# Kernel optimization log

Hardware: AMD Instinct MI355X
Metric: run time of the kernel (lower is better)

The kernel has to match this reference:

```python
import jax, jax.numpy as jnp
import numpy as np

B, K, M, D = 2048, 64, 64, 256
NI, EPS, MI = 15, 0.05, 3


def setup_inputs() -> dict:
    key = jax.random.key(0)
    ks = jax.random.split(key, 8)
    sq = jax.random.normal(ks[0], (B, K, D), dtype=jnp.float32)
    sr = jax.random.normal(ks[1], (B, M, D), dtype=jnp.float32)
    mq = jax.random.uniform(ks[2], (B, K), dtype=jnp.float32)
    mr = jax.random.uniform(ks[3], (B, M), dtype=jnp.float32)
    scale = 1.0 / np.sqrt(D)
    W1 = jax.random.normal(ks[4], (D, D), dtype=jnp.float32) * scale
    b1 = jnp.zeros((D,), dtype=jnp.float32)
    W2 = jax.random.normal(ks[5], (D, D), dtype=jnp.float32) * scale
    b2 = jnp.zeros((D,), dtype=jnp.float32)
    return {"sq": sq, "sr": sr, "mq": mq, "mr": mr,
            "W1": W1, "b1": b1, "W2": W2, "b2": b2}


def _mlp(x, W1, b1, W2, b2):
    # nn.Linear: x @ W.T + b
    h = jax.nn.relu(jnp.einsum('bnd,ed->bne', x, W1) + b1)
    return jnp.einsum('bnd,ed->bne', h, W2) + b2


def _cdist(x, y):
    # Euclidean pairwise distance [B,K,M]
    x2 = jnp.sum(x * x, -1)[:, :, None]
    y2 = jnp.sum(y * y, -1)[:, None, :]
    xy = jnp.einsum('bkd,bmd->bkm', x, y)
    return jnp.sqrt(jnp.clip(x2 + y2 - 2.0 * xy, 0.0))


def reference(sq, sr, mq, mr, W1, b1, W2, b2):
    fq = _mlp(sq, W1, b1, W2, b2)
    fr = _mlp(sr, W1, b1, W2, b2)
    C = _cdist(fq, fr)                                   # [B,K,M]
    lK = (-C / EPS
          + jnp.log(jnp.clip(mq, 1e-8))[:, :, None]
          + jnp.log(jnp.clip(mr, 1e-8))[:, None, :])

    la0 = jnp.zeros((B, K, 1), dtype=C.dtype)
    lb0 = jnp.zeros((B, 1, M), dtype=C.dtype)

    def sink_body(_, carry):
        la, lb = carry
        la = -jax.nn.logsumexp(lK + lb, axis=2, keepdims=True)
        lb = -jax.nn.logsumexp(lK + la, axis=1, keepdims=True)
        return (la, lb)

    la, lb = jax.lax.fori_loop(0, NI, sink_body, (la0, lb0))
    T = jnp.exp(lK + la + lb)

    def pow_body(_, T):
        T = T * T
        T = T / (jnp.sum(T, -1, keepdims=True) + 1e-8)
        T = T / (jnp.sum(T, -2, keepdims=True) + 1e-8)
        return T

    T = jax.lax.fori_loop(0, MI, pow_body, T)
    c = jnp.sum(T * C, axis=(-1, -2))                    # [B]
    return (jax.nn.sigmoid(-c), T, C, c)
```

## Files before the change

### kernel.cpp

```cpp
#include <hip/hip_runtime.h>
#include <math.h>

#define NB    2048
#define KK    64
#define MM    64
#define DD    256
#define NITER 15
#define MITER 3
#define IEPS  20.0f

typedef __bf16 bf16_t;
typedef bf16_t bf16x8 __attribute__((ext_vector_type(8)));
typedef bf16_t bf16x4 __attribute__((ext_vector_type(4)));
typedef float  f32x16 __attribute__((ext_vector_type(16)));

#define XSTR 264
#define CSTR 65

#define F_BYTES   134217728ull
#define WBF_ELEMS 131072

__global__ __launch_bounds__(256) void convert_w(const float* __restrict__ W1,
                                                 const float* __restrict__ W2,
                                                 bf16_t* __restrict__ wbf) {
    int i = blockIdx.x * 256 + threadIdx.x;
    if (i < 65536) wbf[i] = (bf16_t)W1[i];
    else           wbf[i] = (bf16_t)W2[i - 65536];
}

__device__ __forceinline__ void mlp_layer64(const bf16_t* __restrict__ in,
                                            const bf16_t* __restrict__ W,
                                            const float*  __restrict__ bias,
                                            bf16_t* __restrict__ outLds,
                                            bool relu, int l31, int lh, int wv) {
    #pragma unroll
    for (int etp = 0; etp < 2; ++etp) {
        const int e0 = (wv * 2 + etp) * 32;
        bf16x8 af[16];
        const bf16_t* wrow = W + (size_t)(e0 + l31) * 256 + lh * 8;
        #pragma unroll
        for (int kc = 0; kc < 16; ++kc) af[kc] = *(const bf16x8*)(wrow + kc * 16);

        const bf16_t* x0 = in + (size_t)l31 * XSTR + lh * 8;
        const bf16_t* x1 = x0 + 32 * XSTR;
        f32x16 a[2];
        #pragma unroll
        for (int i = 0; i < 16; ++i) { a[0][i] = 0.0f; a[1][i] = 0.0f; }
        #pragma unroll
        for (int kc = 0; kc < 16; ++kc) {
            bf16x8 bx0 = *(const bf16x8*)(x0 + kc * 16);
            bf16x8 bx1 = *(const bf16x8*)(x1 + kc * 16);
            a[0] = __builtin_amdgcn_mfma_f32_32x32x16_bf16(af[kc], bx0, a[0], 0, 0, 0);
            a[1] = __builtin_amdgcn_mfma_f32_32x32x16_bf16(af[kc], bx1, a[1], 0, 0, 0);
        }
        #pragma unroll
        for (int z = 0; z < 2; ++z) {
            const int n = z * 32 + l31;
            #pragma unroll
            for (int g = 0; g < 4; ++g) {
                const int e = e0 + 8 * g + 4 * lh;
                bf16x4 p;
                #pragma unroll
                for (int rr = 0; rr < 4; ++rr) {
                    float v = a[z][4 * g + rr] + bias[e + rr];
                    if (relu) v = fmaxf(v, 0.0f);
                    p[rr] = (bf16_t)v;
                }
                *(bf16x4*)&outLds[(size_t)n * XSTR + e] = p;
            }
        }
    }
}

__global__ __launch_bounds__(256, 2) void mlp_pair(
    const float* __restrict__ sq, const float* __restrict__ sr,
    const float* __restrict__ b1, const float* __restrict__ b2,
    const bf16_t* __restrict__ wbf, bf16_t* __restrict__ fout) {

    __shared__ bf16_t Xs[64 * XSTR];
    __shared__ bf16_t Hs[64 * XSTR];
    __shared__ float  b1_s[256], b2_s[256];

    const int bi = blockIdx.x;
    const int t  = threadIdx.x;
    const int ln = t & 63;
    const int wv = t >> 6;
    const int l31 = ln & 31;
    const int lh  = ln >> 5;

    const int b = bi >> 1, half = bi & 1;
    const float4* s4 = (const float4*)((half ? sr : sq) + (size_t)b * 64 * 256);

    #pragma unroll
    for (int it = 0; it < 16; ++it) {
        const int i  = t + it * 256;
        const int r  = i >> 6;
        const int c4 = i & 63;
        float4 v = s4[i];
        bf16x4 p;
        p[0] = (bf16_t)v.x; p[1] = (bf16_t)v.y;
        p[2] = (bf16_t)v.z; p[3] = (bf16_t)v.w;
        *(bf16x4*)&Xs[(size_t)r * XSTR + c4 * 4] = p;
    }
    b1_s[t] = b1[t];
    b2_s[t] = b2[t];
    __syncthreads();

    mlp_layer64(Xs, wbf, b1_s, Hs, true, l31, lh, wv);
    __syncthreads();
    mlp_layer64(Hs, wbf + 65536, b2_s, Xs, false, l31, lh, wv);
    __syncthreads();

    bf16_t* fg = fout + (size_t)bi * 64 * 256;
    #pragma unroll
    for (int it = 0; it < 8; ++it) {
        const int i = t + it * 256;
        const int r = i >> 5;
        const int c = i & 31;
        bf16x8 v = *(const bf16x8*)&Xs[(size_t)r * XSTR + c * 8];
        *(bf16x8*)&fg[(size_t)r * 256 + c * 8] = v;
    }
}

__global__ __launch_bounds__(256, 2) void sinkhorn_ot(
    const bf16_t* __restrict__ fg,
    const float* __restrict__ mq, const float* __restrict__ mr,
    float* __restrict__ out) {

    __shared__ __align__(16) char smem[128 * XSTR * 2];
    bf16_t* Fs = (bf16_t*)smem;
    float*  Cs = (float*)smem;
    float*  Ts = (float*)(smem + 64 * CSTR * 4);
    __shared__ float nrm[128];
    __shared__ float lmq_s[64], lmr_s[64], la_s[64], lb_s[64];
    __shared__ float red_s[4];

    const int b  = blockIdx.x;
    const int t  = threadIdx.x;
    const int ln = t & 63;
    const int wv = t >> 6;
    const int l31 = ln & 31;
    const int lh  = ln >> 5;

    {
        const bf16_t* fb = fg + (size_t)b * 128 * 256;
        #pragma unroll
        for (int it = 0; it < 16; ++it) {
            const int i = t + it * 256;
            const int r = i >> 5;
            const int c = i & 31;
            bf16x8 v = *(const bf16x8*)&fb[(size_t)r * 256 + c * 8];
            *(bf16x8*)&Fs[(size_t)r * XSTR + c * 8] = v;
        }
        if (t < 64)        lmq_s[t]      = __logf(fmaxf(mq[(size_t)b * 64 + t], 1e-8f));
        else if (t < 128)  lmr_s[t - 64] = __logf(fmaxf(mr[(size_t)b * 64 + (t - 64)], 1e-8f));
        else if (t < 192)  lb_s[t - 128] = 0.0f;
    }
    __syncthreads();

    {
        const int r  = t >> 1;
        const int hf = t & 1;
        const bf16_t* frow = &Fs[(size_t)r * XSTR + hf * 128];
        float s = 0.0f;
        #pragma unroll
        for (int c = 0; c < 16; ++c) {
            bf16x8 v = *(const bf16x8*)(frow + c * 8);
            #pragma unroll
            for (int j2 = 0; j2 < 8; ++j2) { float f = (float)v[j2]; s = fmaf(f, f, s); }
        }
        s += __shfl_xor(s, 1);
        if (hf == 0) nrm[r] = s;
    }
    __syncthreads();

    float cvv[16];
    int   qbase, mcol;
    {
        const int qt = wv >> 1, rt = wv & 1;
        const bf16_t* qa = &Fs[(size_t)(qt * 32 + l31) * XSTR + lh * 8];
        const bf16_t* ra = &Fs[(size_t)(64 + rt * 32 + l31) * XSTR + lh * 8];
        f32x16 acc;
        #pragma unroll
        for (int i = 0; i < 16; ++i) acc[i] = 0.0f;
        #pragma unroll
        for (int kc = 0; kc < 16; ++kc) {
            bf16x8 av = *(const bf16x8*)(qa + kc * 16);
            bf16x8 bv = *(const bf16x8*)(ra + kc * 16);
            acc = __builtin_amdgcn_mfma_f32_32x32x16_bf16(av, bv, acc, 0, 0, 0);
        }
        float* outC = out + 2048 + (size_t)2048 * 4096 + (size_t)b * 4096;
        mcol = rt * 32 + l31;
        qbase = qt * 32;
        const float nr_m = nrm[64 + mcol];
        #pragma unroll
        for (int g = 0; g < 4; ++g) {
            #pragma unroll
            for (int rr = 0; rr < 4; ++rr) {
                const int q = qbase + 8 * g + 4 * lh + rr;
                float d2 = nrm[q] + nr_m - 2.0f * acc[4 * g + rr];
                float cv = sqrtf(fmaxf(d2, 0.0f));
                cvv[4 * g + rr] = cv;
                outC[q * 64 + mcol] = cv;
            }
        }
    }
    __syncthreads();
    {
        #pragma unroll
        for (int g = 0; g < 4; ++g) {
            #pragma unroll
            for (int rr = 0; rr < 4; ++rr) {
                const int q = qbase + 8 * g + 4 * lh + rr;
                Cs[q * CSTR + mcol] = cvv[4 * g + rr];
            }
        }
    }
    __syncthreads();

    const int ki = t >> 2;
    const int jj = t & 3;
    float rowV[16], colV[16];
    #pragma unroll
    for (int i = 0; i < 16; ++i) {
        const int m2 = jj * 16 + i;
        rowV[i] = fmaf(Cs[ki * CSTR + m2], -IEPS, lmr_s[m2]);
        colV[i] = fmaf(Cs[m2 * CSTR + ki], -IEPS, lmq_s[m2]);
    }
    const float lmq_k = lmq_s[ki];
    const float lmr_m = lmr_s[ki];
    float vals[16];

    for (int it = 0; it < NITER; ++it) {
        float mx = -1e30f;
        #pragma unroll
        for (int i = 0; i < 16; ++i) {
            float v = rowV[i] + lb_s[jj * 16 + i];
            vals[i] = v; mx = fmaxf(mx, v);
        }
        mx = fmaxf(mx, __shfl_xor(mx, 1));
        mx = fmaxf(mx, __shfl_xor(mx, 2));
        float s = 0.0f;
        #pragma unroll
        for (int i = 0; i < 16; ++i) s += __expf(vals[i] - mx);
        s += __shfl_xor(s, 1);
        s += __shfl_xor(s, 2);
        if (jj == 0) la_s[ki] = -(lmq_k + mx + __logf(s));
        __syncthreads();

        mx = -1e30f;
        #pragma unroll
        for (int i = 0; i < 16; ++i) {
            float v = colV[i] + la_s[jj * 16 + i];
            vals[i] = v; mx = fmaxf(mx, v);
        }
        mx = fmaxf(mx, __shfl_xor(mx, 1));
        mx = fmaxf(mx, __shfl_xor(mx, 2));
        s = 0.0f;
        #pragma unroll
        for (int i = 0; i < 16; ++i) s += __expf(vals[i] - mx);
        s += __shfl_xor(s, 1);
        s += __shfl_xor(s, 2);
        if (jj == 0) lb_s[ki] = -(lmr_m + mx + __logf(s));
        __syncthreads();
    }

    {
        const float base = lmq_k + la_s[ki];
        #pragma unroll
        for (int i = 0; i < 16; ++i) {
            const int m2 = jj * 16 + i;
            Ts[ki * CSTR + m2] = __expf(rowV[i] + lb_s[m2] + base);
        }
    }
    __syncthreads();

    for (int pi = 0; pi < MITER; ++pi) {
        float vv[16], rs = 0.0f;
        #pragma unroll
        for (int i = 0; i < 16; ++i) {
            float v = Ts[ki * CSTR + jj * 16 + i];
            v = v * v; vv[i] = v; rs += v;
        }
        rs += __shfl_xor(rs, 1); rs += __shfl_xor(rs, 2);
        float inv = 1.0f / (rs + 1e-8f);
        #pragma unroll
        for (int i = 0; i < 16; ++i) Ts[ki * CSTR + jj * 16 + i] = vv[i] * inv;
        __syncthreads();

        float cs = 0.0f;
        #pragma unroll
        for (int i = 0; i < 16; ++i) { float v = Ts[(jj * 16 + i) * CSTR + ki]; vv[i] = v; cs += v; }
        cs += __shfl_xor(cs, 1); cs += __shfl_xor(cs, 2);
        inv = 1.0f / (cs + 1e-8f);
        #pragma unroll
        for (int i = 0; i < 16; ++i) Ts[(jj * 16 + i) * CSTR + ki] = vv[i] * inv;
        __syncthreads();
    }

    {
        float part = 0.0f;
        float tq[16];
        #pragma unroll
        for (int i = 0; i < 16; ++i) {
            const int m2 = jj * 16 + i;
            float tv = Ts[ki * CSTR + m2];
            tq[i] = tv;
            part = fmaf(tv, Cs[ki * CSTR + m2], part);
        }
        float* outT = out + 2048 + (size_t)b * 4096 + ki * 64 + jj * 16;
        #pragma unroll
        for (int q4 = 0; q4 < 4; ++q4) {
            ((float4*)outT)[q4] = make_float4(tq[4 * q4], tq[4 * q4 + 1],
                                              tq[4 * q4 + 2], tq[4 * q4 + 3]);
        }
        #pragma unroll
        for (int off = 1; off < 64; off <<= 1) part += __shfl_xor(part, off);
        if (ln == 0) red_s[wv] = part;
    }
    __syncthreads();
    if (t == 0) {
        float c = red_s[0] + red_s[1] + red_s[2] + red_s[3];
        out[2048 + (size_t)2 * 2048 * 4096 + b] = c;
        out[b] = 1.0f / (1.0f + __expf(c));
    }
}

__device__ __forceinline__ void mlp_layer128(const bf16_t* __restrict__ in,
                                             const bf16_t* __restrict__ W,
                                             const float*  __restrict__ bias,
                                             bf16_t* __restrict__ outLds,
                                             bool relu, int ln, int wv) {
    const int l31 = ln & 31;
    const int lh  = ln >> 5;
    for (int etp = 0; etp < 2; ++etp) {
        const int e0 = (wv * 2 + etp) * 32;
        bf16x8 af[16];
        const bf16_t* wrow = W + (size_t)(e0 + l31) * 256 + lh * 8;
        #pragma unroll
        for (int kc = 0; kc < 16; ++kc) af[kc] = *(const bf16x8*)(wrow + kc * 16);
        #pragma unroll
        for (int ntp = 0; ntp < 2; ++ntp) {
            const bf16_t* x0 = in + (size_t)(ntp * 64 + l31) * XSTR + lh * 8;
            const bf16_t* x1 = x0 + 32 * XSTR;
            f32x16 a[2];
            #pragma unroll
            for (int i = 0; i < 16; ++i) { a[0][i] = 0.0f; a[1][i] = 0.0f; }
            #pragma unroll
            for (int kc = 0; kc < 16; ++kc) {
                bf16x8 bx0 = *(const bf16x8*)(x0 + kc * 16);
                bf16x8 bx1 = *(const bf16x8*)(x1 + kc * 16);
                a[0] = __builtin_amdgcn_mfma_f32_32x32x16_bf16(af[kc], bx0, a[0], 0, 0, 0);
                a[1] = __builtin_amdgcn_mfma_f32_32x32x16_bf16(af[kc], bx1, a[1], 0, 0, 0);
            }
            #pragma unroll
            for (int z = 0; z < 2; ++z) {
                const int n = ntp * 64 + z * 32 + l31;
                #pragma unroll
                for (int g = 0; g < 4; ++g) {
                    const int e = e0 + 8 * g + 4 * lh;
                    bf16x4 p;
                    #pragma unroll
                    for (int rr = 0; rr < 4; ++rr) {
                        float v = a[z][4 * g + rr] + bias[e + rr];
                        if (relu) v = fmaxf(v, 0.0f);
                        p[rr] = (bf16_t)v;
                    }
                    *(bf16x4*)&outLds[(size_t)n * XSTR + e] = p;
                }
            }
        }
    }
}

__global__ __launch_bounds__(256, 1) void sinkhorn_fused(
    const float* __restrict__ sq, const float* __restrict__ sr,
    const float* __restrict__ mq, const float* __restrict__ mr,
    const float* __restrict__ b1, const float* __restrict__ b2,
    const bf16_t* __restrict__ wbf,
    float* __restrict__ out) {

    __shared__ bf16_t Xs[128 * XSTR];
    __shared__ bf16_t Hs[128 * XSTR];
    __shared__ float  Cs[64 * CSTR];
    __shared__ float  nrm[128];
    __shared__ float  lmq_s[64], lmr_s[64], la_s[64], lb_s[64];
    __shared__ float  b1_s[256], b2_s[256];
    __shared__ float  red_s[4];

    const int b  = blockIdx.x;
    const int t  = threadIdx.x;
    const int ln = t & 63;
    const int wv = t >> 6;
    const int l31 = ln & 31;
    const int lh  = ln >> 5;

    {
        const float4* sq4 = (const float4*)(sq + (size_t)b * KK * DD);
        const float4* sr4 = (const float4*)(sr + (size_t)b * MM * DD);
        for (int i = t; i < 8192; i += 256) {
            const int r  = i >> 6;
            const int c4 = i & 63;
            float4 v = (r < 64) ? sq4[r * 64 + c4] : sr4[(r - 64) * 64 + c4];
            bf16x4 p;
            p[0] = (bf16_t)v.x; p[1] = (bf16_t)v.y;
            p[2] = (bf16_t)v.z; p[3] = (bf16_t)v.w;
            *(bf16x4*)&Xs[(size_t)r * XSTR + c4 * 4] = p;
        }
        b1_s[t] = b1[t];
        b2_s[t] = b2[t];
        if (t < 64)        lmq_s[t]       = __logf(fmaxf(mq[(size_t)b * 64 + t], 1e-8f));
        else if (t < 128)  lmr_s[t - 64]  = __logf(fmaxf(mr[(size_t)b * 64 + (t - 64)], 1e-8f));
        else if (t < 192)  lb_s[t - 128]  = 0.0f;
    }
    __syncthreads();
    mlp_layer128(Xs, wbf, b1_s, Hs, true, ln, wv);
    __syncthreads();
    mlp_layer128(Hs, wbf + 65536, b2_s, Xs, false, ln, wv);
    __syncthreads();
    {
        const int r  = t >> 1;
        const int hf = t & 1;
        const bf16_t* frow = &Xs[(size_t)r * XSTR + hf * 128];
        float s = 0.0f;
        #pragma unroll
        for (int c = 0; c < 16; ++c) {
            bf16x8 v = *(const bf16x8*)(frow + c * 8);
            #pragma unroll
            for (int j2 = 0; j2 < 8; ++j2) { float f = (float)v[j2]; s = fmaf(f, f, s); }
        }
        s += __shfl_xor(s, 1);
        if (hf == 0) nrm[r] = s;
    }
    __syncthreads();
    {
        const int qt = wv >> 1, rt = wv & 1;
        const bf16_t* qa = &Xs[(size_t)(qt * 32 + l31) * XSTR + lh * 8];
        const bf16_t* ra = &Xs[(size_t)(64 + rt * 32 + l31) * XSTR + lh * 8];
        f32x16 acc;
        #pragma unroll
        for (int i = 0; i < 16; ++i) acc[i] = 0.0f;
        #pragma unroll
        for (int kc = 0; kc < 16; ++kc) {
            bf16x8 av = *(const bf16x8*)(qa + kc * 16);
            bf16x8 bv = *(const bf16x8*)(ra + kc * 16);
            acc = __builtin_amdgcn_mfma_f32_32x32x16_bf16(av, bv, acc, 0, 0, 0);
        }
        float* outC = out + 2048 + (size_t)2048 * 4096 + (size_t)b * 4096;
        const int m = rt * 32 + l31;
        const float nr_m = nrm[64 + m];
        #pragma unroll
        for (int g = 0; g < 4; ++g) {
            #pragma unroll
            for (int rr = 0; rr < 4; ++rr) {
                const int q = qt * 32 + 8 * g + 4 * lh + rr;
                float d2 = nrm[q] + nr_m - 2.0f * acc[4 * g + rr];
                float cv = sqrtf(fmaxf(d2, 0.0f));
                Cs[q * CSTR + m] = cv;
                outC[q * 64 + m] = cv;
            }
        }
    }
    __syncthreads();

    const int ki = t >> 2;
    const int jj = t & 3;
    float rowV[16], colV[16];
    #pragma unroll
    for (int i = 0; i < 16; ++i) {
        const int m2 = jj * 16 + i;
        rowV[i] = fmaf(Cs[ki * CSTR + m2], -IEPS, lmr_s[m2]);
        colV[i] = fmaf(Cs[m2 * CSTR + ki], -IEPS, lmq_s[m2]);
    }
    const float lmq_k = lmq_s[ki];
    const float lmr_m = lmr_s[ki];
    float vals[16];

    for (int it = 0; it < NITER; ++it) {
        float mx = -1e30f;
        #pragma unroll
        for (int i = 0; i < 16; ++i) {
            float v = rowV[i] + lb_s[jj * 16 + i];
            vals[i] = v; mx = fmaxf(mx, v);
        }
        mx = fmaxf(mx, __shfl_xor(mx, 1));
        mx = fmaxf(mx, __shfl_xor(mx, 2));
        float s = 0.0f;
        #pragma unroll
        for (int i = 0; i < 16; ++i) s += __expf(vals[i] - mx);
        s += __shfl_xor(s, 1);
        s += __shfl_xor(s, 2);
        if (jj == 0) la_s[ki] = -(lmq_k + mx + __logf(s));
        __syncthreads();

        mx = -1e30f;
        #pragma unroll
        for (int i = 0; i < 16; ++i) {
            float v = colV[i] + la_s[jj * 16 + i];
            vals[i] = v; mx = fmaxf(mx, v);
        }
        mx = fmaxf(mx, __shfl_xor(mx, 1));
        mx = fmaxf(mx, __shfl_xor(mx, 2));
        s = 0.0f;
        #pragma unroll
        for (int i = 0; i < 16; ++i) s += __expf(vals[i] - mx);
        s += __shfl_xor(s, 1);
        s += __shfl_xor(s, 2);
        if (jj == 0) lb_s[ki] = -(lmr_m + mx + __logf(s));
        __syncthreads();
    }

    float* Ts = (float*)Hs;
    {
        const float base = lmq_k + la_s[ki];
        #pragma unroll
        for (int i = 0; i < 16; ++i) {
            const int m2 = jj * 16 + i;
            Ts[ki * CSTR + m2] = __expf(rowV[i] + lb_s[m2] + base);
        }
    }
    __syncthreads();

    for (int pi = 0; pi < MITER; ++pi) {
        float vv[16], rs = 0.0f;
        #pragma unroll
        for (int i = 0; i < 16; ++i) {
            float v = Ts[ki * CSTR + jj * 16 + i];
            v = v * v; vv[i] = v; rs += v;
        }
        rs += __shfl_xor(rs, 1); rs += __shfl_xor(rs, 2);
        float inv = 1.0f / (rs + 1e-8f);
        #pragma unroll
        for (int i = 0; i < 16; ++i) Ts[ki * CSTR + jj * 16 + i] = vv[i] * inv;
        __syncthreads();

        float cs = 0.0f;
        #pragma unroll
        for (int i = 0; i < 16; ++i) { float v = Ts[(jj * 16 + i) * CSTR + ki]; vv[i] = v; cs += v; }
        cs += __shfl_xor(cs, 1); cs += __shfl_xor(cs, 2);
        inv = 1.0f / (cs + 1e-8f);
        #pragma unroll
        for (int i = 0; i < 16; ++i) Ts[(jj * 16 + i) * CSTR + ki] = vv[i] * inv;
        __syncthreads();
    }

    {
        float part = 0.0f;
        float tq[16];
        #pragma unroll
        for (int i = 0; i < 16; ++i) {
            const int m2 = jj * 16 + i;
            float tv = Ts[ki * CSTR + m2];
            tq[i] = tv;
            part = fmaf(tv, Cs[ki * CSTR + m2], part);
        }
        float* outT = out + 2048 + (size_t)b * 4096 + ki * 64 + jj * 16;
        #pragma unroll
        for (int q4 = 0; q4 < 4; ++q4) {
            ((float4*)outT)[q4] = make_float4(tq[4 * q4], tq[4 * q4 + 1],
                                              tq[4 * q4 + 2], tq[4 * q4 + 3]);
        }
        #pragma unroll
        for (int off = 1; off < 64; off <<= 1) part += __shfl_xor(part, off);
        if (ln == 0) red_s[wv] = part;
    }
    __syncthreads();
    if (t == 0) {
        float c = red_s[0] + red_s[1] + red_s[2] + red_s[3];
        out[2048 + (size_t)2 * 2048 * 4096 + b] = c;
        out[b] = 1.0f / (1.0f + __expf(c));
    }
}

extern "C" void kernel_launch(void* const* d_in, const int* in_sizes, int n_in,
                              void* d_out, int out_size, void* d_ws, size_t ws_size,
                              hipStream_t stream) {
    const float* sq = (const float*)d_in[0];
    const float* sr = (const float*)d_in[1];
    const float* mq = (const float*)d_in[2];
    const float* mr = (const float*)d_in[3];
    const float* W1 = (const float*)d_in[4];
    const float* b1 = (const float*)d_in[5];
    const float* W2 = (const float*)d_in[6];
    const float* b2 = (const float*)d_in[7];

    const size_t need = F_BYTES + (size_t)WBF_ELEMS * 2;
    if (ws_size >= need) {
        bf16_t* fbuf = (bf16_t*)d_ws;
        bf16_t* wbf  = (bf16_t*)((char*)d_ws + F_BYTES);
        convert_w<<<512, 256, 0, stream>>>(W1, W2, wbf);
        mlp_pair<<<4096, 256, 0, stream>>>(sq, sr, b1, b2, wbf, fbuf);
        sinkhorn_ot<<<NB, 256, 0, stream>>>(fbuf, mq, mr, (float*)d_out);
    } else {
        bf16_t* wbf = (bf16_t*)d_ws;
        convert_w<<<512, 256, 0, stream>>>(W1, W2, wbf);
        sinkhorn_fused<<<NB, 256, 0, stream>>>(sq, sr, mq, mr, b1, b2, wbf, (float*)d_out);
    }
}
```

Before: 519.0 us.

## Cut LDS use in MLP and Sinkhorn kernels to raise occupancy

```diff
diff --git a/kernel.cpp b/kernel.cpp
--- a/kernel.cpp
+++ b/kernel.cpp
@@ -20,6 +20,7 @@
 #define F_BYTES   134217728ull
 #define WBF_ELEMS 131072
 
+
 __global__ __launch_bounds__(256) void convert_w(const float* __restrict__ W1,
                                                  const float* __restrict__ W2,
                                                  bf16_t* __restrict__ wbf) {
@@ -28,57 +29,12 @@
     else           wbf[i] = (bf16_t)W2[i - 65536];
 }
 
-__device__ __forceinline__ void mlp_layer64(const bf16_t* __restrict__ in,
-                                            const bf16_t* __restrict__ W,
-                                            const float*  __restrict__ bias,
-                                            bf16_t* __restrict__ outLds,
-                                            bool relu, int l31, int lh, int wv) {
-    #pragma unroll
-    for (int etp = 0; etp < 2; ++etp) {
-        const int e0 = (wv * 2 + etp) * 32;
-        bf16x8 af[16];
-        const bf16_t* wrow = W + (size_t)(e0 + l31) * 256 + lh * 8;
-        #pragma unroll
-        for (int kc = 0; kc < 16; ++kc) af[kc] = *(const bf16x8*)(wrow + kc * 16);
-
-        const bf16_t* x0 = in + (size_t)l31 * XSTR + lh * 8;
-        const bf16_t* x1 = x0 + 32 * XSTR;
-        f32x16 a[2];
-        #pragma unroll
-        for (int i = 0; i < 16; ++i) { a[0][i] = 0.0f; a[1][i] = 0.0f; }
-        #pragma unroll
-        for (int kc = 0; kc < 16; ++kc) {
-            bf16x8 bx0 = *(const bf16x8*)(x0 + kc * 16);
-            bf16x8 bx1 = *(const bf16x8*)(x1 + kc * 16);
-            a[0] = __builtin_amdgcn_mfma_f32_32x32x16_bf16(af[kc], bx0, a[0], 0, 0, 0);
-            a[1] = __builtin_amdgcn_mfma_f32_32x32x16_bf16(af[kc], bx1, a[1], 0, 0, 0);
-        }
-        #pragma unroll
-        for (int z = 0; z < 2; ++z) {
-            const int n = z * 32 + l31;
-            #pragma unroll
-            for (int g = 0; g < 4; ++g) {
-                const int e = e0 + 8 * g + 4 * lh;
-                bf16x4 p;
-                #pragma unroll
-                for (int rr = 0; rr < 4; ++rr) {
-                    float v = a[z][4 * g + rr] + bias[e + rr];
-                    if (relu) v = fmaxf(v, 0.0f);
-                    p[rr] = (bf16_t)v;
-                }
-                *(bf16x4*)&outLds[(size_t)n * XSTR + e] = p;
-            }
-        }
-    }
-}
-
-__global__ __launch_bounds__(256, 2) void mlp_pair(
+__global__ __launch_bounds__(256, 4) void mlp_pair(
     const float* __restrict__ sq, const float* __restrict__ sr,
     const float* __restrict__ b1, const float* __restrict__ b2,
-    const bf16_t* __restrict__ wbf, bf16_t* __restrict__ fout) {
+    const bf16_t* __restrict__ wbf, bf16_t* __restrict__ ft) {
 
     __shared__ bf16_t Xs[64 * XSTR];
-    __shared__ bf16_t Hs[64 * XSTR];
     __shared__ float  b1_s[256], b2_s[256];
 
     const int bi = blockIdx.x;
@@ -87,50 +43,126 @@
     const int wv = t >> 6;
     const int l31 = ln & 31;
     const int lh  = ln >> 5;
-
     const int b = bi >> 1, half = bi & 1;
-    const float4* s4 = (const float4*)((half ? sr : sq) + (size_t)b * 64 * 256);
-
+
+    {
+        const float4* s4 = (const float4*)((half ? sr : sq) + (size_t)b * 64 * 256);
+        #pragma unroll
+        for (int it = 0; it < 16; ++it) {
+            const int i  = t + it * 256;
+            const int r  = i >> 6;
+            const int c4 = i & 63;
+            float4 v = s4[i];
+            bf16x4 p;
+            p[0] = (bf16_t)v.x; p[1] = (bf16_t)v.y;
+            p[2] = (bf16_t)v.z; p[3] = (bf16_t)v.w;
+            *(bf16x4*)&Xs[(size_t)r * XSTR + c4 * 4] = p;
+        }
+        b1_s[t] = b1[t];
+        b2_s[t] = b2[t];
+    }
+    __syncthreads();
+
+    bf16x4 hreg[2][2][4];
     #pragma unroll
-    for (int it = 0; it < 16; ++it) {
-        const int i  = t + it * 256;
-        const int r  = i >> 6;
-        const int c4 = i & 63;
-        float4 v = s4[i];
-        bf16x4 p;
-        p[0] = (bf16_t)v.x; p[1] = (bf16_t)v.y;
-        p[2] = (bf16_t)v.z; p[3] = (bf16_t)v.w;
-        *(bf16x4*)&Xs[(size_t)r * XSTR + c4 * 4] = p;
-    }
-    b1_s[t] = b1[t];
-    b2_s[t] = b2[t];
-    __syncthreads();
-
-    mlp_layer64(Xs, wbf, b1_s, Hs, true, l31, lh, wv);
-    __syncthreads();
-    mlp_layer64(Hs, wbf + 65536, b2_s, Xs, false, l31, lh, wv);
-    __syncthreads();
-
-    bf16_t* fg = fout + (size_t)bi * 64 * 256;
+    for (int etp = 0; etp < 2; ++etp) {
+        const int e0 = (wv * 2 + etp) * 32;
+        const bf16_t* wrow = wbf + (size_t)(e0 + l31) * 256 + lh * 8;
+        const bf16_t* x0 = Xs + (size_t)l31 * XSTR + lh * 8;
+        const bf16_t* x1 = x0 + 32 * XSTR;
+        f32x16 a[2];
+        #pragma unroll
+        for (int i = 0; i < 16; ++i) { a[0][i] = 0.0f; a[1][i] = 0.0f; }
+        #pragma unroll
+        for (int kg = 0; kg < 4; ++kg) {
+            bf16x8 af[4];
+            #pragma unroll
+            for (int u = 0; u < 4; ++u) af[u] = *(const bf16x8*)(wrow + (kg * 4 + u) * 16);
+            #pragma unroll
+            for (int u = 0; u < 4; ++u) {
+                const int kc = kg * 4 + u;
+                bf16x8 bx0 = *(const bf16x8*)(x0 + kc * 16);
+                bf16x8 bx1 = *(const bf16x8*)(x1 + kc * 16);
+                a[0] = __builtin_amdgcn_mfma_f32_32x32x16_bf16(af[u], bx0, a[0], 0, 0, 0);
+                a[1] = __builtin_amdgcn_mfma_f32_32x32x16_bf16(af[u], bx1, a[1], 0, 0, 0);
+            }
+        }
+        #pragma unroll
+        for (int z = 0; z < 2; ++z) {
+            #pragma unroll
+            for (int g = 0; g < 4; ++g) {
+                const int e = e0 + 8 * g + 4 * lh;
+                #pragma unroll
+                for (int rr = 0; rr < 4; ++rr) {
+                    float v = a[z][4 * g + rr] + b1_s[e + rr];
+                    hreg[etp][z][g][rr] = (bf16_t)fmaxf(v, 0.0f);
+                }
+            }
+        }
+    }
+    __syncthreads();
+
     #pragma unroll
-    for (int it = 0; it < 8; ++it) {
-        const int i = t + it * 256;
-        const int r = i >> 5;
-        const int c = i & 31;
-        bf16x8 v = *(const bf16x8*)&Xs[(size_t)r * XSTR + c * 8];
-        *(bf16x8*)&fg[(size_t)r * 256 + c * 8] = v;
+    for (int etp = 0; etp < 2; ++etp) {
+        const int e0 = (wv * 2 + etp) * 32;
+        #pragma unroll
+        for (int z = 0; z < 2; ++z) {
+            const int n = z * 32 + l31;
+            #pragma unroll
+            for (int g = 0; g < 4; ++g)
+                *(bf16x4*)&Xs[(size_t)n * XSTR + e0 + 8 * g + 4 * lh] = hreg[etp][z][g];
+        }
+    }
+    __syncthreads();
+
+    const size_t ftb = (size_t)b * 32768;
+    #pragma unroll
+    for (int etp = 0; etp < 2; ++etp) {
+        const int e0 = (wv * 2 + etp) * 32;
+        const bf16_t* wrow = wbf + 65536 + (size_t)(e0 + l31) * 256 + lh * 8;
+        const bf16_t* x0 = Xs + (size_t)l31 * XSTR + lh * 8;
+        const bf16_t* x1 = x0 + 32 * XSTR;
+        f32x16 a[2];
+        #pragma unroll
+        for (int i = 0; i < 16; ++i) { a[0][i] = 0.0f; a[1][i] = 0.0f; }
+        #pragma unroll
+        for (int kg = 0; kg < 4; ++kg) {
+            bf16x8 af[4];
+            #pragma unroll
+            for (int u = 0; u < 4; ++u) af[u] = *(const bf16x8*)(wrow + (kg * 4 + u) * 16);
+            #pragma unroll
+            for (int u = 0; u < 4; ++u) {
+                const int kc = kg * 4 + u;
+                bf16x8 bx0 = *(const bf16x8*)(x0 + kc * 16);
+                bf16x8 bx1 = *(const bf16x8*)(x1 + kc * 16);
+                a[0] = __builtin_amdgcn_mfma_f32_32x32x16_bf16(af[u], bx0, a[0], 0, 0, 0);
+                a[1] = __builtin_amdgcn_mfma_f32_32x32x16_bf16(af[u], bx1, a[1], 0, 0, 0);
+            }
+        }
+        #pragma unroll
+        for (int z = 0; z < 2; ++z) {
+            const int row = half * 64 + z * 32 + l31;
+            #pragma unroll
+            for (int g = 0; g < 4; ++g) {
+                const int e = e0 + 8 * g + 4 * lh;
+                bf16x4 p;
+                #pragma unroll
+                for (int rr = 0; rr < 4; ++rr)
+                    p[rr] = (bf16_t)(a[z][4 * g + rr] + b2_s[e + rr]);
+                const int j = (wv * 2 + etp) * 4 + g;
+                *(bf16x4*)&ft[ftb + ((size_t)j * 128 + row) * 8 + 4 * lh] = p;
+            }
+        }
     }
 }
 
-__global__ __launch_bounds__(256, 2) void sinkhorn_ot(
-    const bf16_t* __restrict__ fg,
+__global__ __launch_bounds__(256, 4) void sinkhorn_ot(
+    const bf16_t* __restrict__ ft,
     const float* __restrict__ mq, const float* __restrict__ mr,
     float* __restrict__ out) {
 
-    __shared__ __align__(16) char smem[128 * XSTR * 2];
-    bf16_t* Fs = (bf16_t*)smem;
-    float*  Cs = (float*)smem;
-    float*  Ts = (float*)(smem + 64 * CSTR * 4);
+    __shared__ float Cs[64 * CSTR];
+    __shared__ float Ts[64 * CSTR];
     __shared__ float nrm[128];
     __shared__ float lmq_s[64], lmr_s[64], la_s[64], lb_s[64];
     __shared__ float red_s[4];
@@ -141,17 +173,21 @@
     const int wv = t >> 6;
     const int l31 = ln & 31;
     const int lh  = ln >> 5;
-
-    {
-        const bf16_t* fb = fg + (size_t)b * 128 * 256;
-        #pragma unroll
-        for (int it = 0; it < 16; ++it) {
-            const int i = t + it * 256;
-            const int r = i >> 5;
-            const int c = i & 31;
-            bf16x8 v = *(const bf16x8*)&fb[(size_t)r * 256 + c * 8];
-            *(bf16x8*)&Fs[(size_t)r * XSTR + c * 8] = v;
-        }
+    const size_t ftb = (size_t)b * 32768;
+
+    {
+        const int r  = t >> 1;
+        const int hf = t & 1;
+        float s = 0.0f;
+        #pragma unroll
+        for (int j2 = 0; j2 < 16; ++j2) {
+            const int j = hf * 16 + j2;
+            bf16x8 v = *(const bf16x8*)&ft[ftb + ((size_t)j * 128 + r) * 8];
+            #pragma unroll
+            for (int u = 0; u < 8; ++u) { float f = (float)v[u]; s = fmaf(f, f, s); }
+        }
+        s += __shfl_xor(s, 1);
+        if (hf == 0) nrm[r] = s;
         if (t < 64)        lmq_s[t]      = __logf(fmaxf(mq[(size_t)b * 64 + t], 1e-8f));
         else if (t < 128)  lmr_s[t - 64] = __logf(fmaxf(mr[(size_t)b * 64 + (t - 64)], 1e-8f));
         else if (t < 192)  lb_s[t - 128] = 0.0f;
@@ -159,60 +195,29 @@
     __syncthreads();
 
     {
-        const int r  = t >> 1;
-        const int hf = t & 1;
-        const bf16_t* frow = &Fs[(size_t)r * XSTR + hf * 128];
-        float s = 0.0f;
-        #pragma unroll
-        for (int c = 0; c < 16; ++c) {
-            bf16x8 v = *(const bf16x8*)(frow + c * 8);
-            #pragma unroll
-            for (int j2 = 0; j2 < 8; ++j2) { float f = (float)v[j2]; s = fmaf(f, f, s); }
-        }
-        s += __shfl_xor(s, 1);
-        if (hf == 0) nrm[r] = s;
-    }
-    __syncthreads();
-
-    float cvv[16];
-    int   qbase, mcol;
-    {
         const int qt = wv >> 1, rt = wv & 1;
-        const bf16_t* qa = &Fs[(size_t)(qt * 32 + l31) * XSTR + lh * 8];
-        const bf16_t* ra = &Fs[(size_t)(64 + rt * 32 + l31) * XSTR + lh * 8];
         f32x16 acc;
         #pragma unroll
         for (int i = 0; i < 16; ++i) acc[i] = 0.0f;
         #pragma unroll
         for (int kc = 0; kc < 16; ++kc) {
-            bf16x8 av = *(const bf16x8*)(qa + kc * 16);
-            bf16x8 bv = *(const bf16x8*)(ra + kc * 16);
+            const size_t jb = ftb + (size_t)(2 * kc + lh) * 1024;
+            bf16x8 av = *(const bf16x8*)&ft[jb + (qt * 32 + l31) * 8];
+            bf16x8 bv = *(const bf16x8*)&ft[jb + (64 + rt * 32 + l31) * 8];
             acc = __builtin_amdgcn_mfma_f32_32x32x16_bf16(av, bv, acc, 0, 0, 0);
         }
+        const int m = rt * 32 + l31;
+        const float nr_m = nrm[64 + m];
         float* outC = out + 2048 + (size_t)2048 * 4096 + (size_t)b * 4096;
-        mcol = rt * 32 + l31;
-        qbase = qt * 32;
-        const float nr_m = nrm[64 + mcol];
         #pragma unroll
         for (int g = 0; g < 4; ++g) {
             #pragma unroll
             for (int rr = 0; rr < 4; ++rr) {
-                const int q = qbase + 8 * g + 4 * lh + rr;
+                const int q = qt * 32 + 8 * g + 4 * lh + rr;
                 float d2 = nrm[q] + nr_m - 2.0f * acc[4 * g + rr];
                 float cv = sqrtf(fmaxf(d2, 0.0f));
-                cvv[4 * g + rr] = cv;
-                outC[q * 64 + mcol] = cv;
-            }
-        }
-    }
-    __syncthreads();
-    {
-        #pragma unroll
-        for (int g = 0; g < 4; ++g) {
-            #pragma unroll
-            for (int rr = 0; rr < 4; ++rr) {
-                const int q = qbase + 8 * g + 4 * lh + rr;
-                Cs[q * CSTR + mcol] = cvv[4 * g + rr];
+                Cs[q * CSTR + m] = cv;
+                outC[q * 64 + m] = cv;
             }
         }
     }
@@ -229,20 +234,16 @@
     }
     const float lmq_k = lmq_s[ki];
     const float lmr_m = lmr_s[ki];
-    float vals[16];
 
     for (int it = 0; it < NITER; ++it) {
         float mx = -1e30f;
         #pragma unroll
-        for (int i = 0; i < 16; ++i) {
-            float v = rowV[i] + lb_s[jj * 16 + i];
-            vals[i] = v; mx = fmaxf(mx, v);
-        }
+        for (int i = 0; i < 16; ++i) mx = fmaxf(mx, rowV[i] + lb_s[jj * 16 + i]);
         mx = fmaxf(mx, __shfl_xor(mx, 1));
         mx = fmaxf(mx, __shfl_xor(mx, 2));
         float s = 0.0f;
         #pragma unroll
-        for (int i = 0; i < 16; ++i) s += __expf(vals[i] - mx);
+        for (int i = 0; i < 16; ++i) s += __expf(rowV[i] + lb_s[jj * 16 + i] - mx);
         s += __shfl_xor(s, 1);
         s += __shfl_xor(s, 2);
         if (jj == 0) la_s[ki] = -(lmq_k + mx + __logf(s));
@@ -250,15 +251,12 @@
 
         mx = -1e30f;
         #pragma unroll
-        for (int i = 0; i < 16; ++i) {
-            float v = colV[i] + la_s[jj * 16 + i];
-            vals[i] = v; mx = fmaxf(mx, v);
-        }
+        for (int i = 0; i < 16; ++i) mx = fmaxf(mx, colV[i] + la_s[jj * 16 + i]);
         mx = fmaxf(mx, __shfl_xor(mx, 1));
         mx = fmaxf(mx, __shfl_xor(mx, 2));
         s = 0.0f;
         #pragma unroll
-        for (int i = 0; i < 16; ++i) s += __expf(vals[i] - mx);
+        for (int i = 0; i < 16; ++i) s += __expf(colV[i] + la_s[jj * 16 + i] - mx);
         s += __shfl_xor(s, 1);
         s += __shfl_xor(s, 2);
         if (jj == 0) lb_s[ki] = -(lmr_m + mx + __logf(s));
@@ -474,20 +472,16 @@
     }
     const float lmq_k = lmq_s[ki];
     const float lmr_m = lmr_s[ki];
-    float vals[16];
 
     for (int it = 0; it < NITER; ++it) {
         float mx = -1e30f;
         #pragma unroll
-        for (int i = 0; i < 16; ++i) {
-            float v = rowV[i] + lb_s[jj * 16 + i];
-            vals[i] = v; mx = fmaxf(mx, v);
-        }
+        for (int i = 0; i < 16; ++i) mx = fmaxf(mx, rowV[i] + lb_s[jj * 16 + i]);
         mx = fmaxf(mx, __shfl_xor(mx, 1));
         mx = fmaxf(mx, __shfl_xor(mx, 2));
         float s = 0.0f;
         #pragma unroll
-        for (int i = 0; i < 16; ++i) s += __expf(vals[i] - mx);
+        for (int i = 0; i < 16; ++i) s += __expf(rowV[i] + lb_s[jj * 16 + i] - mx);
         s += __shfl_xor(s, 1);
         s += __shfl_xor(s, 2);
         if (jj == 0) la_s[ki] = -(lmq_k + mx + __logf(s));
@@ -495,15 +489,12 @@
 
         mx = -1e30f;
         #pragma unroll
-        for (int i = 0; i < 16; ++i) {
-            float v = colV[i] + la_s[jj * 16 + i];
-            vals[i] = v; mx = fmaxf(mx, v);
-        }
+        for (int i = 0; i < 16; ++i) mx = fmaxf(mx, colV[i] + la_s[jj * 16 + i]);
         mx = fmaxf(mx, __shfl_xor(mx, 1));
         mx = fmaxf(mx, __shfl_xor(mx, 2));
         s = 0.0f;
         #pragma unroll
-        for (int i = 0; i < 16; ++i) s += __expf(vals[i] - mx);
+        for (int i = 0; i < 16; ++i) s += __expf(colV[i] + la_s[jj * 16 + i] - mx);
         s += __shfl_xor(s, 1);
         s += __shfl_xor(s, 2);
         if (jj == 0) lb_s[ki] = -(lmr_m + mx + __logf(s));
```

Result: faster. 502.2 us (-3.3%).
